# Optimization experiments

Measured on AMD Instinct MI355X. Metric: run time of the kernel, lower is better.

The kernel has to match this reference:

```python
import jax, jax.numpy as jnp
import numpy as np

IN_FEATURES = 128
OUT_FEATURES = 64
NEG_INF = -9e15
LEAKY_SLOPE = 0.01  # nn.LeakyReLU() default


def _xavier_uniform(key, shape, gain):
    fan_in, fan_out = shape[0], shape[1]
    limit = gain * np.sqrt(6.0 / (fan_in + fan_out))
    return jax.random.uniform(key, shape, jnp.float32, -limit, limit)


def setup_inputs() -> dict:
    key = jax.random.key(0)
    k_h, k_adj, k_w, k_a = jax.random.split(key, 4)
    B, N = 8, 2048
    h = jax.random.normal(k_h, (B, N, IN_FEATURES), dtype=jnp.float32)
    adj = jax.random.randint(k_adj, (B, N, N), 0, 2, dtype=jnp.int32)
    W = _xavier_uniform(k_w, (IN_FEATURES, OUT_FEATURES), gain=1.414)
    a = _xavier_uniform(k_a, (2 * OUT_FEATURES, 1), gain=1.414)
    return {"h": h, "adj": adj, "W": W, "a": a}


def reference(h, adj, W, a):
    # Wh: [B, N, out]
    Wh = jnp.matmul(h, W)
    # a1, a2: [out, 1] slices of a
    a1 = a[:OUT_FEATURES]
    a2 = a[OUT_FEATURES:]
    Wh_a1 = jnp.matmul(Wh, a1)  # [B, N, 1]
    Wh_a2 = jnp.matmul(Wh, a2)  # [B, N, 1]
    # e[b,i,j] = leakyrelu(Wh_a1[b,i] * Wh_a2[b,j])  -- rank-1 outer product
    e = jax.nn.leaky_relu(Wh_a1 * jnp.swapaxes(Wh_a2, 1, 2), negative_slope=LEAKY_SLOPE)
    mask = adj > 0
    attention = jnp.where(mask, e, NEG_INF)
    attention = jax.nn.softmax(attention, axis=2)
    attention = jnp.where(mask, attention, 0.0)
    h_prime = jnp.matmul(attention, Wh)  # [B, N, out]
    return jax.nn.elu(h_prime)  # concat=True
```

## Files before the change

### kernel.cpp

```cpp
#include <hip/hip_runtime.h>

#define NTOK 2048

typedef __attribute__((ext_vector_type(8))) short s8v;
typedef __attribute__((ext_vector_type(4))) float f32x4;

__device__ inline unsigned short f2bf(float f) {
  unsigned u = __builtin_bit_cast(unsigned, f);
  u += 0x7FFFu + ((u >> 16) & 1u);
  return (unsigned short)(u >> 16);
}

__global__ __launch_bounds__(256) void gat_pre(
    const float* __restrict__ h, const float* __restrict__ W,
    const float* __restrict__ a, unsigned short* __restrict__ WhT,
    float* __restrict__ f1, float* __restrict__ f2,
    float* __restrict__ gmaxs, float* __restrict__ gmins) {
  __shared__ float wL[128 * 64];
  __shared__ float hL[64 * 128];
  __shared__ unsigned short tL[64 * 66];
  __shared__ float bmx[4], bmn[4];
  int t = threadIdx.x;
  {
    const float4* W4 = (const float4*)W;
    float4* wL4 = (float4*)wL;
#pragma unroll
    for (int k = 0; k < 8; ++k) wL4[t + 256 * k] = W4[t + 256 * k];
    const float4* h4 = (const float4*)(h + (size_t)blockIdx.x * 64 * 128);
    float4* hL4 = (float4*)hL;
#pragma unroll
    for (int k = 0; k < 8; ++k) hL4[t + 256 * k] = h4[t + 256 * k];
  }
  __syncthreads();
  int w = t >> 6, lane = t & 63;
  float acc[16];
#pragma unroll
  for (int r = 0; r < 16; ++r) acc[r] = 0.f;
  for (int kc = 0; kc < 128; kc += 32) {
    float wreg[32];
#pragma unroll
    for (int kk = 0; kk < 32; ++kk) wreg[kk] = wL[(kc + kk) * 64 + lane];
#pragma unroll
    for (int r = 0; r < 16; ++r) {
      const float* hrow = &hL[(w * 16 + r) * 128 + kc];
#pragma unroll
      for (int kk = 0; kk < 32; kk += 4) {
        float4 hv = *(const float4*)(hrow + kk);
        acc[r] += hv.x * wreg[kk] + hv.y * wreg[kk + 1] +
                  hv.z * wreg[kk + 2] + hv.w * wreg[kk + 3];
      }
    }
  }
  float a1 = a[lane], a2 = a[lane + 64];
  int row0 = blockIdx.x * 64 + w * 16;
  float wmx = -3.4e38f, wmn = 3.4e38f;
#pragma unroll
  for (int r = 0; r < 16; ++r) {
    float v1 = acc[r] * a1, v2 = acc[r] * a2;
#pragma unroll
    for (int s = 32; s; s >>= 1) {
      v1 += __shfl_xor(v1, s, 64);
      v2 += __shfl_xor(v2, s, 64);
    }
    if (lane == 0) { f1[row0 + r] = v1; f2[row0 + r] = v2; }
    wmx = fmaxf(wmx, v2);
    wmn = fminf(wmn, v2);
    tL[lane * 66 + w * 16 + r] = f2bf(acc[r]);
  }
  if (lane == 0) { bmx[w] = wmx; bmn[w] = wmn; }
  __syncthreads();
  int b = blockIdx.x >> 5;
  if (t == 0) {
    float mx = fmaxf(fmaxf(bmx[0], bmx[1]), fmaxf(bmx[2], bmx[3]));
    float mn = fminf(fminf(bmn[0], bmn[1]), fminf(bmn[2], bmn[3]));
    gmaxs[b * 32 + (blockIdx.x & 31)] = mx;
    gmins[b * 32 + (blockIdx.x & 31)] = mn;
  }
  int tok0 = (blockIdx.x & 31) * 64;
  int f = t >> 2, sub = t & 3;
  const unsigned short* src = &tL[f * 66];
  unsigned short* dst = WhT + ((size_t)b * 64 + f) * NTOK + tok0;
  *(uint4*)(dst + sub * 8) = *(const uint4*)(src + sub * 8);
  *(uint4*)(dst + 32 + sub * 8) = *(const uint4*)(src + 32 + sub * 8);
}

#define LOADX4(dst, va) \
  asm volatile("global_load_dwordx4 %0, %1, off" : "=v"(dst) : "v"(va))
#define WAITV(n) \
  asm volatile("s_waitcnt vmcnt(" #n ")" ::: "memory"); \
  __builtin_amdgcn_sched_barrier(0)
#define PACK4(s0, s1, s2, s3, s4, s5, s6, s7, D)                               \
  {                                                                            \
    unsigned b0 = (unsigned)(s0.x > 0) | ((unsigned)(s0.y > 0) << 1) |         \
                  ((unsigned)(s0.z > 0) << 2) | ((unsigned)(s0.w > 0) << 3) |  \
                  ((unsigned)(s1.x > 0) << 4) | ((unsigned)(s1.y > 0) << 5) |  \
                  ((unsigned)(s1.z > 0) << 6) | ((unsigned)(s1.w > 0) << 7);   \
    unsigned b1 = (unsigned)(s2.x > 0) | ((unsigned)(s2.y > 0) << 1) |         \
                  ((unsigned)(s2.z > 0) << 2) | ((unsigned)(s2.w > 0) << 3) |  \
                  ((unsigned)(s3.x > 0) << 4) | ((unsigned)(s3.y > 0) << 5) |  \
                  ((unsigned)(s3.z > 0) << 6) | ((unsigned)(s3.w > 0) << 7);   \
    unsigned b2 = (unsigned)(s4.x > 0) | ((unsigned)(s4.y > 0) << 1) |         \
                  ((unsigned)(s4.z > 0) << 2) | ((unsigned)(s4.w > 0) << 3) |  \
                  ((unsigned)(s5.x > 0) << 4) | ((unsigned)(s5.y > 0) << 5) |  \
                  ((unsigned)(s5.z > 0) << 6) | ((unsigned)(s5.w > 0) << 7);   \
    unsigned b3 = (unsigned)(s6.x > 0) | ((unsigned)(s6.y > 0) << 1) |         \
                  ((unsigned)(s6.z > 0) << 2) | ((unsigned)(s6.w > 0) << 3) |  \
                  ((unsigned)(s7.x > 0) << 4) | ((unsigned)(s7.y > 0) << 5) |  \
                  ((unsigned)(s7.z > 0) << 6) | ((unsigned)(s7.w > 0) << 7);   \
    D = b0 | (b1 << 8) | (b2 << 16) | (b3 << 24);                              \
  }

__global__ __launch_bounds__(512, 2) void gat_main(
    const int* __restrict__ adj, const unsigned short* __restrict__ WhT,
    const float* __restrict__ f1, const float* __restrict__ f2,
    const float* __restrict__ gmaxs, const float* __restrict__ gmins,
    unsigned short* __restrict__ part, float* __restrict__ dsum) {
  __shared__ __align__(16) unsigned char wTile[65536];
  __shared__ float f2L[512];
  __shared__ __align__(16) unsigned char mT[8][1024];
  int t = threadIdx.x;
  int pt = blockIdx.x, b = blockIdx.y, ks = blockIdx.z;
  int w = t >> 6, lane = t & 63, l15 = lane & 15, lhi = lane >> 4;

  {
    int ff = t >> 3;
    const char* srow =
        (const char*)(WhT + (size_t)b * 64 * NTOK + (size_t)ff * NTOK + ks * 512);
    int cb0 = (t & 7) * 128;
#pragma unroll
    for (int u = 0; u < 8; ++u) {
      int cb = cb0 + u * 16;
      uint4 d = *(const uint4*)(srow + cb);
      *(uint4*)&wTile[ff * 1024 + (cb ^ ((ff & 7) << 4))] = d;
    }
    if (t < 128)
      ((float4*)f2L)[t] = ((const float4*)(f2 + (size_t)b * NTOK + ks * 512))[t];
  }
  __syncthreads();

  int rg = pt * 8 + w;
  int i0 = rg * 16;
  const float L2E = 1.44269504f;
  float f1s = f1[(size_t)b * NTOK + i0 + l15] * L2E;
  float gmx = -3.4e38f, gmn = 3.4e38f;
#pragma unroll
  for (int j = 0; j < 32; ++j) {
    gmx = fmaxf(gmx, gmaxs[b * 32 + j]);
    gmn = fminf(gmn, gmins[b * 32 + j]);
  }
  float mr = fmaxf(f1s * gmx, f1s * gmn);
  float ms = fmaxf(mr, 0.01f * mr);

  unsigned d0, d1, d2, d3;
  {
    const int* abase = adj + ((size_t)b * NTOK + i0) * NTOK + ks * 512;
    unsigned long long bp = (unsigned long long)abase + (unsigned)(lane * 32);
    int4 A0, A1, A2, A3, A4, A5, A6, A7;
    int4 B0, B1, B2, B3, B4, B5, B6, B7;
    __builtin_amdgcn_sched_barrier(0);
    LOADX4(A0, bp + 0ull);       LOADX4(A1, bp + 16ull);
    LOADX4(A2, bp + 8192ull);    LOADX4(A3, bp + 8208ull);
    LOADX4(A4, bp + 16384ull);   LOADX4(A5, bp + 16400ull);
    LOADX4(A6, bp + 24576ull);   LOADX4(A7, bp + 24592ull);
    LOADX4(B0, bp + 32768ull);   LOADX4(B1, bp + 32784ull);
    LOADX4(B2, bp + 40960ull);   LOADX4(B3, bp + 40976ull);
    LOADX4(B4, bp + 49152ull);   LOADX4(B5, bp + 49168ull);
    LOADX4(B6, bp + 57344ull);   LOADX4(B7, bp + 57360ull);
    WAITV(8);
    PACK4(A0, A1, A2, A3, A4, A5, A6, A7, d0);
    LOADX4(A0, bp + 65536ull);   LOADX4(A1, bp + 65552ull);
    LOADX4(A2, bp + 73728ull);   LOADX4(A3, bp + 73744ull);
    LOADX4(A4, bp + 81920ull);   LOADX4(A5, bp + 81936ull);
    LOADX4(A6, bp + 90112ull);   LOADX4(A7, bp + 90128ull);
    WAITV(8);
    PACK4(B0, B1, B2, B3, B4, B5, B6, B7, d1);
    LOADX4(B0, bp + 98304ull);   LOADX4(B1, bp + 98320ull);
    LOADX4(B2, bp + 106496ull);  LOADX4(B3, bp + 106512ull);
    LOADX4(B4, bp + 114688ull);  LOADX4(B5, bp + 114704ull);
    LOADX4(B6, bp + 122880ull);  LOADX4(B7, bp + 122896ull);
    WAITV(8);
    PACK4(A0, A1, A2, A3, A4, A5, A6, A7, d2);
    WAITV(0);
    PACK4(B0, B1, B2, B3, B4, B5, B6, B7, d3);
    __builtin_amdgcn_sched_barrier(0);
  }

  {
    uint4 dd = {d0, d1, d2, d3};
    *(uint4*)&mT[w][lane * 16] = dd;
  }

  const s8v bones = {0x3F80, 0x3F80, 0x3F80, 0x3F80, 0x3F80, 0x3F80, 0x3F80, 0x3F80};
  f32x4 ac0 = {0.f, 0.f, 0.f, 0.f}, ac1 = ac0, ac2 = ac0, ac3 = ac0, ac4 = ac0;
  int sw = (l15 & 7) << 4;

#pragma unroll
  for (int ch = 0; ch < 16; ++ch) {
    unsigned byte = mT[w][(ch * 4 + lhi) * 16 + l15];
    float4 v0 = *(const float4*)&f2L[ch * 32 + lhi * 8];
    float4 v1 = *(const float4*)&f2L[ch * 32 + lhi * 8 + 4];
    int kb = ch * 64 + lhi * 16;
    s8v bf0 = *(const s8v*)&wTile[l15 * 1024 + (kb ^ sw)];
    s8v bf1 = *(const s8v*)&wTile[(16 + l15) * 1024 + (kb ^ sw)];
    s8v bf2 = *(const s8v*)&wTile[(32 + l15) * 1024 + (kb ^ sw)];
    s8v bf3 = *(const s8v*)&wTile[(48 + l15) * 1024 + (kb ^ sw)];

    float sv[8] = {f1s * v0.x, f1s * v0.y, f1s * v0.z, f1s * v0.w,
                   f1s * v1.x, f1s * v1.y, f1s * v1.z, f1s * v1.w};
    s8v af;
#pragma unroll
    for (int q = 0; q < 8; ++q) {
      float sc = sv[q];
      float lk = fmaxf(sc, 0.01f * sc);
#if __has_builtin(__builtin_amdgcn_exp2f)
      float pe = __builtin_amdgcn_exp2f(lk - ms);
#else
      float pe = exp2f(lk - ms);
#endif
      float p = (byte & (1u << q)) ? pe : 0.f;
      unsigned uu = __builtin_bit_cast(unsigned, p) + 0x8000u;
      af[q] = (short)(uu >> 16);
    }
    ac0 = __builtin_amdgcn_mfma_f32_16x16x32_bf16(af, bf0, ac0, 0, 0, 0);
    ac1 = __builtin_amdgcn_mfma_f32_16x16x32_bf16(af, bf1, ac1, 0, 0, 0);
    ac2 = __builtin_amdgcn_mfma_f32_16x16x32_bf16(af, bf2, ac2, 0, 0, 0);
    ac3 = __builtin_amdgcn_mfma_f32_16x16x32_bf16(af, bf3, ac3, 0, 0, 0);
    ac4 = __builtin_amdgcn_mfma_f32_16x16x32_bf16(af, bones, ac4, 0, 0, 0);
  }

  size_t pb = ((size_t)(b * 128 + rg)) * 4 + ks;
  unsigned short* pp = part + pb * 1024;
#pragma unroll
  for (int reg = 0; reg < 4; ++reg) {
    int row = lhi * 4 + reg;
    pp[row * 64 + l15] = f2bf(ac0[reg]);
    pp[row * 64 + 16 + l15] = f2bf(ac1[reg]);
    pp[row * 64 + 32 + l15] = f2bf(ac2[reg]);
    pp[row * 64 + 48 + l15] = f2bf(ac3[reg]);
    if (l15 == 0) dsum[pb * 16 + row] = ac4[reg];
  }
}

__global__ __launch_bounds__(256) void gat_fin(
    const unsigned short* __restrict__ part, const float* __restrict__ dsum,
    float* __restrict__ out) {
  int gx = blockIdx.x, b = blockIdx.y, t = threadIdx.x;
  size_t g = (size_t)b * 128 + gx;
#pragma unroll
  for (int rep = 0; rep < 4; ++rep) {
    int idx = t + rep * 256;
    int mm = idx >> 6, f = idx & 63;
    float v = 0.f, dn = 0.f;
#pragma unroll
    for (int ks = 0; ks < 4; ++ks) {
      size_t pb = g * 4 + ks;
      unsigned us = part[pb * 1024 + mm * 64 + f];
      v += __builtin_bit_cast(float, us << 16);
      dn += dsum[pb * 16 + mm];
    }
    float rdn = dn > 0.f ? 1.0f / dn : 0.f;
    float hp = v * rdn;
    float o = hp > 0.f ? hp : expm1f(hp);
    out[((size_t)b * NTOK + gx * 16 + mm) * 64 + f] = o;
  }
}

extern "C" void kernel_launch(void* const* d_in, const int* in_sizes, int n_in,
                              void* d_out, int out_size, void* d_ws, size_t ws_size,
                              hipStream_t stream) {
  const float* h = (const float*)d_in[0];
  const int* adj = (const int*)d_in[1];
  const float* W = (const float*)d_in[2];
  const float* a = (const float*)d_in[3];
  float* out = (float*)d_out;

  char* ws = (char*)d_ws;
  unsigned short* WhT = (unsigned short*)ws;
  float* f1 = (float*)(ws + 2 * 1024 * 1024);
  float* f2 = f1 + 16384;
  float* gmaxs = (float*)(f2 + 16384);
  float* gmins = gmaxs + 256;
  unsigned short* part = (unsigned short*)(ws + 3 * 1024 * 1024);
  float* dsum = (float*)(ws + 11 * 1024 * 1024);

  gat_pre<<<256, 256, 0, stream>>>(h, W, a, WhT, f1, f2, gmaxs, gmins);
  gat_main<<<dim3(16, 8, 4), 512, 0, stream>>>(adj, WhT, f1, f2, gmaxs, gmins,
                                               part, dsum);
  gat_fin<<<dim3(128, 8), 256, 0, stream>>>(part, dsum, out);
}
```

Measured before the change: 57.74 us.

## Fuse finalize into main kernel with in-block split-K reduction over row tiles

The main kernel now has each block own 16 output rows across all 2048 columns. The eight waves split the columns among themselves and reduce their partial accumulators in shared memory, then apply normalisation and ELU directly. This removes the separate finalize kernel and the bf16 partial/dsum round trip through global memory. In exchange, the WhT tile is reloaded four times per block with extra barriers, and each block now streams a 16-row adjacency tile with a different load pattern.

```diff
diff --git a/kernel.cpp b/kernel.cpp
--- a/kernel.cpp
+++ b/kernel.cpp
@@ -89,57 +89,30 @@
 #define WAITV(n) \
   asm volatile("s_waitcnt vmcnt(" #n ")" ::: "memory"); \
   __builtin_amdgcn_sched_barrier(0)
-#define PACK4(s0, s1, s2, s3, s4, s5, s6, s7, D)                               \
-  {                                                                            \
-    unsigned b0 = (unsigned)(s0.x > 0) | ((unsigned)(s0.y > 0) << 1) |         \
-                  ((unsigned)(s0.z > 0) << 2) | ((unsigned)(s0.w > 0) << 3) |  \
-                  ((unsigned)(s1.x > 0) << 4) | ((unsigned)(s1.y > 0) << 5) |  \
-                  ((unsigned)(s1.z > 0) << 6) | ((unsigned)(s1.w > 0) << 7);   \
-    unsigned b1 = (unsigned)(s2.x > 0) | ((unsigned)(s2.y > 0) << 1) |         \
-                  ((unsigned)(s2.z > 0) << 2) | ((unsigned)(s2.w > 0) << 3) |  \
-                  ((unsigned)(s3.x > 0) << 4) | ((unsigned)(s3.y > 0) << 5) |  \
-                  ((unsigned)(s3.z > 0) << 6) | ((unsigned)(s3.w > 0) << 7);   \
-    unsigned b2 = (unsigned)(s4.x > 0) | ((unsigned)(s4.y > 0) << 1) |         \
-                  ((unsigned)(s4.z > 0) << 2) | ((unsigned)(s4.w > 0) << 3) |  \
-                  ((unsigned)(s5.x > 0) << 4) | ((unsigned)(s5.y > 0) << 5) |  \
-                  ((unsigned)(s5.z > 0) << 6) | ((unsigned)(s5.w > 0) << 7);   \
-    unsigned b3 = (unsigned)(s6.x > 0) | ((unsigned)(s6.y > 0) << 1) |         \
-                  ((unsigned)(s6.z > 0) << 2) | ((unsigned)(s6.w > 0) << 3) |  \
-                  ((unsigned)(s7.x > 0) << 4) | ((unsigned)(s7.y > 0) << 5) |  \
-                  ((unsigned)(s7.z > 0) << 6) | ((unsigned)(s7.w > 0) << 7);   \
-    D = b0 | (b1 << 8) | (b2 << 16) | (b3 << 24);                              \
+#define PKB(Xa, Xb, D)                                                        \
+  {                                                                           \
+    int4 pa = Xa;                                                             \
+    int4 pq = Xb;                                                             \
+    D = (unsigned)(pa.x > 0) | ((unsigned)(pa.y > 0) << 1) |                  \
+        ((unsigned)(pa.z > 0) << 2) | ((unsigned)(pa.w > 0) << 3) |           \
+        ((unsigned)(pq.x > 0) << 4) | ((unsigned)(pq.y > 0) << 5) |           \
+        ((unsigned)(pq.z > 0) << 6) | ((unsigned)(pq.w > 0) << 7);            \
   }
 
 __global__ __launch_bounds__(512, 2) void gat_main(
     const int* __restrict__ adj, const unsigned short* __restrict__ WhT,
     const float* __restrict__ f1, const float* __restrict__ f2,
     const float* __restrict__ gmaxs, const float* __restrict__ gmins,
-    unsigned short* __restrict__ part, float* __restrict__ dsum) {
+    float* __restrict__ out) {
   __shared__ __align__(16) unsigned char wTile[65536];
-  __shared__ float f2L[512];
-  __shared__ __align__(16) unsigned char mT[8][1024];
+  __shared__ __align__(16) unsigned char mT[16 * 260];
+  __shared__ float f2L[2048];
+  __shared__ float sums[8 * 16];
   int t = threadIdx.x;
-  int pt = blockIdx.x, b = blockIdx.y, ks = blockIdx.z;
+  int b = blockIdx.y;
+  int i0 = blockIdx.x * 16;
   int w = t >> 6, lane = t & 63, l15 = lane & 15, lhi = lane >> 4;
 
-  {
-    int ff = t >> 3;
-    const char* srow =
-        (const char*)(WhT + (size_t)b * 64 * NTOK + (size_t)ff * NTOK + ks * 512);
-    int cb0 = (t & 7) * 128;
-#pragma unroll
-    for (int u = 0; u < 8; ++u) {
-      int cb = cb0 + u * 16;
-      uint4 d = *(const uint4*)(srow + cb);
-      *(uint4*)&wTile[ff * 1024 + (cb ^ ((ff & 7) << 4))] = d;
-    }
-    if (t < 128)
-      ((float4*)f2L)[t] = ((const float4*)(f2 + (size_t)b * NTOK + ks * 512))[t];
-  }
-  __syncthreads();
-
-  int rg = pt * 8 + w;
-  int i0 = rg * 16;
   const float L2E = 1.44269504f;
   float f1s = f1[(size_t)b * NTOK + i0 + l15] * L2E;
   float gmx = -3.4e38f, gmn = 3.4e38f;
@@ -151,117 +124,142 @@
   float mr = fmaxf(f1s * gmx, f1s * gmn);
   float ms = fmaxf(mr, 0.01f * mr);
 
-  unsigned d0, d1, d2, d3;
+  int ff = t >> 3;
+  int cb0 = (t & 7) * 128;
+  int swf = (ff & 7) << 4;
+  const char* wsrc = (const char*)(WhT + (size_t)b * 64 * NTOK);
+
   {
-    const int* abase = adj + ((size_t)b * NTOK + i0) * NTOK + ks * 512;
-    unsigned long long bp = (unsigned long long)abase + (unsigned)(lane * 32);
-    int4 A0, A1, A2, A3, A4, A5, A6, A7;
-    int4 B0, B1, B2, B3, B4, B5, B6, B7;
+    int4 S0, S1, S2, S3, S4, S5, S6, S7, F0;
+    int4 G0, G1, G2, G3, G4, G5, G6, G7;
+    int4 G8, G9, G10, G11, G12, G13, G14, G15;
+    unsigned long long sb = (unsigned long long)(wsrc) + (unsigned)(ff * 4096 + cb0);
+    unsigned long long fb = (unsigned long long)(f2 + (size_t)b * NTOK) + (unsigned)(t * 16);
+    unsigned long long r0 =
+        (unsigned long long)(adj + ((size_t)b * NTOK + i0 + 2 * w) * NTOK) +
+        (unsigned)(lane * 32);
     __builtin_amdgcn_sched_barrier(0);
-    LOADX4(A0, bp + 0ull);       LOADX4(A1, bp + 16ull);
-    LOADX4(A2, bp + 8192ull);    LOADX4(A3, bp + 8208ull);
-    LOADX4(A4, bp + 16384ull);   LOADX4(A5, bp + 16400ull);
-    LOADX4(A6, bp + 24576ull);   LOADX4(A7, bp + 24592ull);
-    LOADX4(B0, bp + 32768ull);   LOADX4(B1, bp + 32784ull);
-    LOADX4(B2, bp + 40960ull);   LOADX4(B3, bp + 40976ull);
-    LOADX4(B4, bp + 49152ull);   LOADX4(B5, bp + 49168ull);
-    LOADX4(B6, bp + 57344ull);   LOADX4(B7, bp + 57360ull);
+    LOADX4(S0, sb + 0ull);    LOADX4(S1, sb + 16ull);
+    LOADX4(S2, sb + 32ull);   LOADX4(S3, sb + 48ull);
+    LOADX4(S4, sb + 64ull);   LOADX4(S5, sb + 80ull);
+    LOADX4(S6, sb + 96ull);   LOADX4(S7, sb + 112ull);
+    LOADX4(F0, fb);
+    LOADX4(G0, r0 + 0ull);      LOADX4(G1, r0 + 16ull);
+    LOADX4(G2, r0 + 8192ull);   LOADX4(G3, r0 + 8208ull);
+    LOADX4(G4, r0 + 2048ull);   LOADX4(G5, r0 + 2064ull);
+    LOADX4(G6, r0 + 10240ull);  LOADX4(G7, r0 + 10256ull);
+    LOADX4(G8, r0 + 4096ull);   LOADX4(G9, r0 + 4112ull);
+    LOADX4(G10, r0 + 12288ull); LOADX4(G11, r0 + 12304ull);
+    LOADX4(G12, r0 + 6144ull);  LOADX4(G13, r0 + 6160ull);
+    LOADX4(G14, r0 + 14336ull); LOADX4(G15, r0 + 14352ull);
+    WAITV(16);
+    *(int4*)&wTile[ff * 1024 + ((cb0 + 0) ^ swf)] = S0;
+    *(int4*)&wTile[ff * 1024 + ((cb0 + 16) ^ swf)] = S1;
+    *(int4*)&wTile[ff * 1024 + ((cb0 + 32) ^ swf)] = S2;
+    *(int4*)&wTile[ff * 1024 + ((cb0 + 48) ^ swf)] = S3;
+    *(int4*)&wTile[ff * 1024 + ((cb0 + 64) ^ swf)] = S4;
+    *(int4*)&wTile[ff * 1024 + ((cb0 + 80) ^ swf)] = S5;
+    *(int4*)&wTile[ff * 1024 + ((cb0 + 96) ^ swf)] = S6;
+    *(int4*)&wTile[ff * 1024 + ((cb0 + 112) ^ swf)] = S7;
+    *(int4*)&f2L[t * 4] = F0;
+    int ra = 2 * w, rb = 2 * w + 1;
+    unsigned by;
+    WAITV(12);
+    PKB(G0, G1, by);   mT[ra * 260 + 0 * 64 + lane] = (unsigned char)by;
+    PKB(G2, G3, by);   mT[rb * 260 + 0 * 64 + lane] = (unsigned char)by;
     WAITV(8);
-    PACK4(A0, A1, A2, A3, A4, A5, A6, A7, d0);
-    LOADX4(A0, bp + 65536ull);   LOADX4(A1, bp + 65552ull);
-    LOADX4(A2, bp + 73728ull);   LOADX4(A3, bp + 73744ull);
-    LOADX4(A4, bp + 81920ull);   LOADX4(A5, bp + 81936ull);
-    LOADX4(A6, bp + 90112ull);   LOADX4(A7, bp + 90128ull);
-    WAITV(8);
-    PACK4(B0, B1, B2, B3, B4, B5, B6, B7, d1);
-    LOADX4(B0, bp + 98304ull);   LOADX4(B1, bp + 98320ull);
-    LOADX4(B2, bp + 106496ull);  LOADX4(B3, bp + 106512ull);
-    LOADX4(B4, bp + 114688ull);  LOADX4(B5, bp + 114704ull);
-    LOADX4(B6, bp + 122880ull);  LOADX4(B7, bp + 122896ull);
-    WAITV(8);
-    PACK4(A0, A1, A2, A3, A4, A5, A6, A7, d2);
+    PKB(G4, G5, by);   mT[ra * 260 + 1 * 64 + lane] = (unsigned char)by;
+    PKB(G6, G7, by);   mT[rb * 260 + 1 * 64 + lane] = (unsigned char)by;
+    WAITV(4);
+    PKB(G8, G9, by);   mT[ra * 260 + 2 * 64 + lane] = (unsigned char)by;
+    PKB(G10, G11, by); mT[rb * 260 + 2 * 64 + lane] = (unsigned char)by;
     WAITV(0);
-    PACK4(B0, B1, B2, B3, B4, B5, B6, B7, d3);
+    PKB(G12, G13, by); mT[ra * 260 + 3 * 64 + lane] = (unsigned char)by;
+    PKB(G14, G15, by); mT[rb * 260 + 3 * 64 + lane] = (unsigned char)by;
     __builtin_amdgcn_sched_barrier(0);
   }
-
-  {
-    uint4 dd = {d0, d1, d2, d3};
-    *(uint4*)&mT[w][lane * 16] = dd;
-  }
+  __syncthreads();
 
   const s8v bones = {0x3F80, 0x3F80, 0x3F80, 0x3F80, 0x3F80, 0x3F80, 0x3F80, 0x3F80};
   f32x4 ac0 = {0.f, 0.f, 0.f, 0.f}, ac1 = ac0, ac2 = ac0, ac3 = ac0, ac4 = ac0;
   int sw = (l15 & 7) << 4;
 
 #pragma unroll
-  for (int ch = 0; ch < 16; ++ch) {
-    unsigned byte = mT[w][(ch * 4 + lhi) * 16 + l15];
-    float4 v0 = *(const float4*)&f2L[ch * 32 + lhi * 8];
-    float4 v1 = *(const float4*)&f2L[ch * 32 + lhi * 8 + 4];
-    int kb = ch * 64 + lhi * 16;
-    s8v bf0 = *(const s8v*)&wTile[l15 * 1024 + (kb ^ sw)];
-    s8v bf1 = *(const s8v*)&wTile[(16 + l15) * 1024 + (kb ^ sw)];
-    s8v bf2 = *(const s8v*)&wTile[(32 + l15) * 1024 + (kb ^ sw)];
-    s8v bf3 = *(const s8v*)&wTile[(48 + l15) * 1024 + (kb ^ sw)];
-
-    float sv[8] = {f1s * v0.x, f1s * v0.y, f1s * v0.z, f1s * v0.w,
-                   f1s * v1.x, f1s * v1.y, f1s * v1.z, f1s * v1.w};
-    s8v af;
-#pragma unroll
-    for (int q = 0; q < 8; ++q) {
-      float sc = sv[q];
-      float lk = fmaxf(sc, 0.01f * sc);
+  for (int ks = 0; ks < 4; ++ks) {
+    if (ks > 0) {
+      __syncthreads();
+#pragma unroll
+      for (int u = 0; u < 8; ++u) {
+        int cb = cb0 + u * 16;
+        uint4 d = *(const uint4*)(wsrc + (size_t)ff * 4096 + ks * 1024 + cb);
+        *(uint4*)&wTile[ff * 1024 + (cb ^ swf)] = d;
+      }
+      __syncthreads();
+    }
+#pragma unroll
+    for (int cc = 0; cc < 2; ++cc) {
+      int c = w * 2 + cc;
+      unsigned byte = mT[l15 * 260 + ks * 64 + c * 4 + lhi];
+      const float* fv = &f2L[ks * 512 + c * 32 + lhi * 8];
+      float4 v0 = *(const float4*)(fv);
+      float4 v1 = *(const float4*)(fv + 4);
+      int kb = c * 64 + lhi * 16;
+      s8v bf0 = *(const s8v*)&wTile[l15 * 1024 + (kb ^ sw)];
+      s8v bf1 = *(const s8v*)&wTile[(16 + l15) * 1024 + (kb ^ sw)];
+      s8v bf2 = *(const s8v*)&wTile[(32 + l15) * 1024 + (kb ^ sw)];
+      s8v bf3 = *(const s8v*)&wTile[(48 + l15) * 1024 + (kb ^ sw)];
+
+      float sv[8] = {f1s * v0.x, f1s * v0.y, f1s * v0.z, f1s * v0.w,
+                     f1s * v1.x, f1s * v1.y, f1s * v1.z, f1s * v1.w};
+      s8v af;
+#pragma unroll
+      for (int q = 0; q < 8; ++q) {
+        float sc = sv[q];
+        float lk = fmaxf(sc, 0.01f * sc);
 #if __has_builtin(__builtin_amdgcn_exp2f)
-      float pe = __builtin_amdgcn_exp2f(lk - ms);
+        float pe = __builtin_amdgcn_exp2f(lk - ms);
 #else
-      float pe = exp2f(lk - ms);
+        float pe = exp2f(lk - ms);
 #endif
-      float p = (byte & (1u << q)) ? pe : 0.f;
-      unsigned uu = __builtin_bit_cast(unsigned, p) + 0x8000u;
-      af[q] = (short)(uu >> 16);
-    }
-    ac0 = __builtin_amdgcn_mfma_f32_16x16x32_bf16(af, bf0, ac0, 0, 0, 0);
-    ac1 = __builtin_amdgcn_mfma_f32_16x16x32_bf16(af, bf1, ac1, 0, 0, 0);
-    ac2 = __builtin_amdgcn_mfma_f32_16x16x32_bf16(af, bf2, ac2, 0, 0, 0);
-    ac3 = __builtin_amdgcn_mfma_f32_16x16x32_bf16(af, bf3, ac3, 0, 0, 0);
-    ac4 = __builtin_amdgcn_mfma_f32_16x16x32_bf16(af, bones, ac4, 0, 0, 0);
-  }
-
-  size_t pb = ((size_t)(b * 128 + rg)) * 4 + ks;
-  unsigned short* pp = part + pb * 1024;
+        float p = (byte & (1u << q)) ? pe : 0.f;
+        unsigned uu = __builtin_bit_cast(unsigned, p) + 0x8000u;
+        af[q] = (short)(uu >> 16);
+      }
+      ac0 = __builtin_amdgcn_mfma_f32_16x16x32_bf16(af, bf0, ac0, 0, 0, 0);
+      ac1 = __builtin_amdgcn_mfma_f32_16x16x32_bf16(af, bf1, ac1, 0, 0, 0);
+      ac2 = __builtin_amdgcn_mfma_f32_16x16x32_bf16(af, bf2, ac2, 0, 0, 0);
+      ac3 = __builtin_amdgcn_mfma_f32_16x16x32_bf16(af, bf3, ac3, 0, 0, 0);
+      ac4 = __builtin_amdgcn_mfma_f32_16x16x32_bf16(af, bones, ac4, 0, 0, 0);
+    }
+  }
+
+  __syncthreads();
+  float* red = (float*)wTile;
 #pragma unroll
   for (int reg = 0; reg < 4; ++reg) {
     int row = lhi * 4 + reg;
-    pp[row * 64 + l15] = f2bf(ac0[reg]);
-    pp[row * 64 + 16 + l15] = f2bf(ac1[reg]);
-    pp[row * 64 + 32 + l15] = f2bf(ac2[reg]);
-    pp[row * 64 + 48 + l15] = f2bf(ac3[reg]);
-    if (l15 == 0) dsum[pb * 16 + row] = ac4[reg];
-  }
-}
-
-__global__ __launch_bounds__(256) void gat_fin(
-    const unsigned short* __restrict__ part, const float* __restrict__ dsum,
-    float* __restrict__ out) {
-  int gx = blockIdx.x, b = blockIdx.y, t = threadIdx.x;
-  size_t g = (size_t)b * 128 + gx;
-#pragma unroll
-  for (int rep = 0; rep < 4; ++rep) {
-    int idx = t + rep * 256;
+    float* dst = &red[w * 1088 + row * 68 + l15];
+    dst[0] = ac0[reg];
+    dst[16] = ac1[reg];
+    dst[32] = ac2[reg];
+    dst[48] = ac3[reg];
+    if (l15 == 0) sums[w * 16 + row] = ac4[reg];
+  }
+  __syncthreads();
+#pragma unroll
+  for (int rep = 0; rep < 2; ++rep) {
+    int idx = t + rep * 512;
     int mm = idx >> 6, f = idx & 63;
     float v = 0.f, dn = 0.f;
 #pragma unroll
-    for (int ks = 0; ks < 4; ++ks) {
-      size_t pb = g * 4 + ks;
-      unsigned us = part[pb * 1024 + mm * 64 + f];
-      v += __builtin_bit_cast(float, us << 16);
-      dn += dsum[pb * 16 + mm];
+    for (int w2 = 0; w2 < 8; ++w2) {
+      v += red[w2 * 1088 + mm * 68 + f];
+      dn += sums[w2 * 16 + mm];
     }
     float rdn = dn > 0.f ? 1.0f / dn : 0.f;
     float hp = v * rdn;
     float o = hp > 0.f ? hp : expm1f(hp);
-    out[((size_t)b * NTOK + gx * 16 + mm) * 64 + f] = o;
+    out[((size_t)b * NTOK + i0 + mm) * 64 + f] = o;
   }
 }
 
@@ -280,11 +278,7 @@
   float* f2 = f1 + 16384;
   float* gmaxs = (float*)(f2 + 16384);
   float* gmins = gmaxs + 256;
-  unsigned short* part = (unsigned short*)(ws + 3 * 1024 * 1024);
-  float* dsum = (float*)(ws + 11 * 1024 * 1024);
 
   gat_pre<<<256, 256, 0, stream>>>(h, W, a, WhT, f1, f2, gmaxs, gmins);
-  gat_main<<<dim3(16, 8, 4), 512, 0, stream>>>(adj, WhT, f1, f2, gmaxs, gmins,
-                                               part, dsum);
-  gat_fin<<<dim3(128, 8), 256, 0, stream>>>(part, dsum, out);
-}
+  gat_main<<<dim3(128, 8), 512, 0, stream>>>(adj, WhT, f1, f2, gmaxs, gmins, out);
+}
```

Measured after the change: 77.02 us. 1.33x slower.
